# Kernel tuning notes

Measured on AMD Instinct MI355X. Metric: run time of the kernel, lower is better.

## Reference

```python
import jax, jax.numpy as jnp
import numpy as np

B, L, D = 4, 64, 512          # batch, trajectory length, d_model
DI, N, DC, R = 1024, 16, 4, 32  # d_inner, d_state, d_conv, dt_rank
NL = 4                         # n_layers
SD, AD, MEL = 17, 6, 1000      # state_dim, act_dim, max_ep_len
EPS = 1e-5


def setup_inputs() -> dict:
    key = jax.random.key(0)
    ks = iter(jax.random.split(key, 40))
    nrm = lambda shp, s=0.02: jax.random.normal(next(ks), shp, jnp.float32) * s
    inp = {
        "states": jax.random.normal(next(ks), (B, L, SD), jnp.float32),
        "actions": jax.random.normal(next(ks), (B, L, AD), jnp.float32),
        "returns_to_go": jax.random.normal(next(ks), (B, L, 1), jnp.float32),
        "constraints_to_go": jax.random.normal(next(ks), (B, L, 1), jnp.float32),
        "timesteps": jax.random.randint(next(ks), (B, L), 0, MEL, jnp.int32),
        # embedding / projection heads (torch Linear: y = x @ W.T + b)
        "es_w": nrm((D, SD)), "es_b": jnp.zeros((D,), jnp.float32),
        "ea_w": nrm((D, AD)), "ea_b": jnp.zeros((D,), jnp.float32),
        "er_w": nrm((D, 1)), "er_b": jnp.zeros((D,), jnp.float32),
        "ec_w": nrm((D, 1)), "ec_b": jnp.zeros((D,), jnp.float32),
        "et_w": nrm((MEL, D)),
        # per-layer Mamba params, stacked on leading NL axis
        "ln_w": jnp.ones((NL, D), jnp.float32), "ln_b": jnp.zeros((NL, D), jnp.float32),
        "in_w": nrm((NL, 2 * DI, D)),
        "conv_w": nrm((NL, DI, DC), 0.1), "conv_b": jnp.zeros((NL, DI), jnp.float32),
        "xp_w": nrm((NL, R + 2 * N, DI)),
        "dtp_w": nrm((NL, DI, R), 0.1),
        "dtp_b": jnp.full((NL, DI), -4.6, jnp.float32) + nrm((NL, DI), 0.1),
        "A_log": jnp.broadcast_to(jnp.log(jnp.arange(1, N + 1, dtype=jnp.float32)), (NL, DI, N)) * jnp.ones((NL, DI, 1), jnp.float32),
        "Dp": jnp.ones((NL, DI), jnp.float32),
        "out_w": nrm((NL, D, DI)),
        # final norm + heads
        "fn_w": jnp.ones((D,), jnp.float32), "fn_b": jnp.zeros((D,), jnp.float32),
        "ps_w": nrm((SD, D)), "ps_b": jnp.zeros((SD,), jnp.float32),
        "pa_w": nrm((AD, D)), "pa_b": jnp.zeros((AD,), jnp.float32),
    }
    return inp


def layernorm(x, w, b):
    mu = jnp.mean(x, -1, keepdims=True)
    var = jnp.mean(jnp.square(x - mu), -1, keepdims=True)
    return (x - mu) * jax.lax.rsqrt(var + EPS) * w + b


def selective_scan(u, delta, A, Bm, Cm, Dp):
    # u, delta: (B,T,DI); A: (DI,N); Bm, Cm: (B,T,N); Dp: (DI,)
    dA = jnp.exp(delta[..., None] * A)                      # (B,T,DI,N)
    dBu = delta[..., None] * Bm[:, :, None, :] * u[..., None]

    def step(h, xs):
        dA_t, dBu_t, C_t = xs
        h = dA_t * h + dBu_t                                # (B,DI,N)
        y = jnp.einsum('bdn,bn->bd', h, C_t)
        return h, y

    h0 = jnp.zeros((u.shape[0], u.shape[2], A.shape[1]), u.dtype)
    xs = (dA.transpose(1, 0, 2, 3), dBu.transpose(1, 0, 2, 3), Cm.transpose(1, 0, 2))
    _, ys = jax.lax.scan(step, h0, xs)
    return ys.transpose(1, 0, 2) + u * Dp


def mamba_mixer(x, in_w, conv_w, conv_b, xp_w, dtp_w, dtp_b, A_log, Dp, out_w):
    T = x.shape[1]
    xz = x @ in_w.T                                         # (B,T,2*DI)
    xm, z = jnp.split(xz, 2, axis=-1)
    # causal depthwise conv1d, kernel DC
    xpad = jnp.pad(xm, ((0, 0), (DC - 1, 0), (0, 0)))
    xc = sum(xpad[:, k:k + T, :] * conv_w[:, k] for k in range(DC)) + conv_b
    xc = jax.nn.silu(xc)
    dbc = xc @ xp_w.T                                       # (B,T,R+2N)
    dt, Bm, Cm = jnp.split(dbc, [R, R + N], axis=-1)
    delta = jax.nn.softplus(dt @ dtp_w.T + dtp_b)           # (B,T,DI)
    y = selective_scan(xc, delta, -jnp.exp(A_log), Bm, Cm, Dp)
    y = y * jax.nn.silu(z)
    return y @ out_w.T


def reference(states, actions, returns_to_go, constraints_to_go, timesteps,
              es_w, es_b, ea_w, ea_b, er_w, er_b, ec_w, ec_b, et_w,
              ln_w, ln_b, in_w, conv_w, conv_b, xp_w, dtp_w, dtp_b, A_log, Dp, out_w,
              fn_w, fn_b, ps_w, ps_b, pa_w, pa_b):
    te = et_w[timesteps]                                    # (B,L,D)
    se = states @ es_w.T + es_b + te
    ae = actions @ ea_w.T + ea_b + te
    re = returns_to_go @ er_w.T + er_b + te
    ce = constraints_to_go @ ec_w.T + ec_b + te
    # interleave (r, c, s, a) per timestep -> (B, 4L, D)
    x = jnp.stack((re, ce, se, ae), axis=2).reshape(B, 4 * L, D)
    for i in range(NL):
        x = x + mamba_mixer(layernorm(x, ln_w[i], ln_b[i]),
                            in_w[i], conv_w[i], conv_b[i], xp_w[i],
                            dtp_w[i], dtp_b[i], A_log[i], Dp[i], out_w[i])
    x = layernorm(x, fn_w, fn_b)
    outputs = x.reshape(B, L, 4, D).transpose(0, 2, 1, 3)   # (B,4,L,D)
    state_preds = outputs[:, 3] @ ps_w.T + ps_b             # from action tokens
    action_preds = outputs[:, 2] @ pa_w.T + pa_b            # from state tokens
    return state_preds, action_preds
```

## Files before the change

kernel.cpp:

```cpp
#include <hip/hip_runtime.h>
#include <math.h>

#define B_ 4
#define L_ 64
#define D_ 512
#define DI_ 1024
#define N_ 16
#define DC_ 4
#define R_ 32
#define NL_ 4
#define SD_ 17
#define AD_ 6
#define T_ 256
#define CH3_ 32
#define TC3_ 8
#define DL3_ 8

#define NW_IN  (NL_ * 2 * DI_ * D_)
#define NW_OUT (NL_ * D_ * DI_)
#define NW_XP  (NL_ * 64 * DI_)
#define NW_TOT (NW_IN + NW_OUT + NW_XP)
#define WCVT_BLOCKS (NW_TOT / 4 / 256)

typedef short bf16x8 __attribute__((ext_vector_type(8)));
typedef float f32x4 __attribute__((ext_vector_type(4)));

__device__ __forceinline__ float silu_f(float v) { return v / (1.f + __expf(-v)); }
__device__ __forceinline__ float softplus_f(float v) {
    return fmaxf(v, 0.f) + log1pf(__expf(-fabsf(v)));
}
__device__ __forceinline__ unsigned short f2bs(float f) {
    unsigned u = __float_as_uint(f);
    u += 0x7fffu + ((u >> 16) & 1u);
    return (unsigned short)(u >> 16);
}
__device__ __forceinline__ float bs2f(unsigned short s) {
    return __uint_as_float(((unsigned)s) << 16);
}

__global__ __launch_bounds__(256) void init_kernel(
    const float* __restrict__ in_w, const float* __restrict__ out_w,
    const float* __restrict__ xp_w, unsigned short* __restrict__ wb,
    const float* __restrict__ states, const float* __restrict__ actions,
    const float* __restrict__ rtg, const float* __restrict__ ctg,
    const int* __restrict__ ts,
    const float* __restrict__ es_w, const float* __restrict__ es_b,
    const float* __restrict__ ea_w, const float* __restrict__ ea_b,
    const float* __restrict__ er_w, const float* __restrict__ er_b,
    const float* __restrict__ ec_w, const float* __restrict__ ec_b,
    const float* __restrict__ et_w, float* __restrict__ x)
{
    if (blockIdx.x < WCVT_BLOCKS) {
        const int i = blockIdx.x * 256 + threadIdx.x;
        const int e = i * 4;
        const float* src; int off;
        if (e < NW_IN)               { src = in_w;  off = e; }
        else if (e < NW_IN + NW_OUT) { src = out_w; off = e - NW_IN; }
        else                         { src = xp_w;  off = e - NW_IN - NW_OUT; }
        const float4 v = *(const float4*)(src + off);
        ushort4 o;
        o.x = f2bs(v.x); o.y = f2bs(v.y); o.z = f2bs(v.z); o.w = f2bs(v.w);
        *(ushort4*)(wb + e) = o;
    } else {
        const int bl = blockIdx.x - WCVT_BLOCKS;
#pragma unroll
        for (int j = 0; j < 2; ++j) {
            const int d = threadIdx.x + j * 256;
            const float te = et_w[(size_t)ts[bl] * D_ + d];
            const float r = rtg[bl] * er_w[d] + er_b[d] + te;
            const float c = ctg[bl] * ec_w[d] + ec_b[d] + te;
            float s = es_b[d] + te;
#pragma unroll
            for (int k = 0; k < SD_; ++k) s += states[bl * SD_ + k] * es_w[d * SD_ + k];
            float a = ea_b[d] + te;
#pragma unroll
            for (int k = 0; k < AD_; ++k) a += actions[bl * AD_ + k] * ea_w[d * AD_ + k];
            float* xp = x + (size_t)bl * 4 * D_;
            xp[0 * D_ + d] = r;
            xp[1 * D_ + d] = c;
            xp[2 * D_ + d] = s;
            xp[3 * D_ + d] = a;
        }
    }
}

template <int MODE>
__global__ __launch_bounds__(256) void ln2_kernel(
    float* __restrict__ x, const float* __restrict__ p0,
    const float* __restrict__ p1,
    const float* __restrict__ w, const float* __restrict__ b,
    void* __restrict__ o_)
{
    const int tok = blockIdx.x;
    const int tid = threadIdx.x;
    float2 v = reinterpret_cast<float2*>(x + (size_t)tok * D_)[tid];
    if (MODE >= 1) {
        const float2 a0 = reinterpret_cast<const float2*>(p0 + (size_t)tok * D_)[tid];
        const float2 a1 = reinterpret_cast<const float2*>(p1 + (size_t)tok * D_)[tid];
        v.x += a0.x + a1.x;
        v.y += a0.y + a1.y;
        reinterpret_cast<float2*>(x + (size_t)tok * D_)[tid] = v;
    }
    float s = v.x + v.y;
#pragma unroll
    for (int off = 1; off < 64; off <<= 1) s += __shfl_xor(s, off);
    __shared__ float red[8];
    const int wv = tid >> 6;
    if ((tid & 63) == 0) red[wv] = s;
    __syncthreads();
    const float mean = (red[0] + red[1] + red[2] + red[3]) * (1.f / D_);
    const float dx = v.x - mean, dy = v.y - mean;
    float q = dx * dx + dy * dy;
#pragma unroll
    for (int off = 1; off < 64; off <<= 1) q += __shfl_xor(q, off);
    if ((tid & 63) == 0) red[4 + wv] = q;
    __syncthreads();
    const float var = (red[4] + red[5] + red[6] + red[7]) * (1.f / D_);
    const float r = rsqrtf(var + 1e-5f);
    const int d0 = tid * 2;
    const float o0 = dx * r * w[d0] + b[d0];
    const float o1 = dy * r * w[d0 + 1] + b[d0 + 1];
    if (MODE == 2) {
        float* o = (float*)o_;
        o[(size_t)tok * D_ + d0] = o0;
        o[(size_t)tok * D_ + d0 + 1] = o1;
    } else {
        unsigned short* o = (unsigned short*)o_;
        o[(size_t)tok * D_ + d0] = f2bs(o0);
        o[(size_t)tok * D_ + d0 + 1] = f2bs(o1);
    }
}

__global__ __launch_bounds__(256) void inproj_kernel(
    const unsigned short* __restrict__ A, const unsigned short* __restrict__ W,
    const float* __restrict__ cw, const float* __restrict__ cb,
    unsigned short* __restrict__ xcb, unsigned short* __restrict__ zs)
{
    __shared__ unsigned short sxm[80][72];
    const int lane = threadIdx.x & 63, wid = threadIdx.x >> 6;
    const int r = lane & 15, kq = lane >> 4;
    const int m0 = blockIdx.y * 64;
    const int n0 = blockIdx.x * 64;
    const bool is_xm = (n0 < DI_);
    const int wm = m0 + (wid >> 1) * 32;
    const int wn = n0 + (wid & 1) * 32;
    f32x4 acc[2][2] = {};
    f32x4 accx[2] = {};
    int xrow = m0 - 16 + r;
    if (xrow < 0) xrow = 0;
#pragma unroll 4
    for (int k0 = 0; k0 < D_; k0 += 32) {
        bf16x8 a[2], b[2];
#pragma unroll
        for (int i = 0; i < 2; ++i)
            a[i] = *(const bf16x8*)(A + (size_t)(wm + i * 16 + r) * D_ + k0 + kq * 8);
#pragma unroll
        for (int j = 0; j < 2; ++j)
            b[j] = *(const bf16x8*)(W + (size_t)(wn + j * 16 + r) * D_ + k0 + kq * 8);
#pragma unroll
        for (int i = 0; i < 2; ++i)
#pragma unroll
            for (int j = 0; j < 2; ++j)
                acc[i][j] = __builtin_amdgcn_mfma_f32_16x16x32_bf16(a[i], b[j], acc[i][j], 0, 0, 0);
        if (is_xm) {
            const bf16x8 ax = *(const bf16x8*)(A + (size_t)xrow * D_ + k0 + kq * 8);
#pragma unroll
            for (int j = 0; j < 2; ++j)
                accx[j] = __builtin_amdgcn_mfma_f32_16x16x32_bf16(ax, b[j], accx[j], 0, 0, 0);
        }
    }
    if (!is_xm) {
#pragma unroll
        for (int i = 0; i < 2; ++i)
#pragma unroll
            for (int j = 0; j < 2; ++j)
#pragma unroll
                for (int g = 0; g < 4; ++g) {
                    const int row = wm + i * 16 + kq * 4 + g;
                    const int col = wn + j * 16 + r - DI_;
                    zs[(size_t)row * DI_ + col] = f2bs(silu_f(acc[i][j][g]));
                }
        return;
    }
#pragma unroll
    for (int i = 0; i < 2; ++i)
#pragma unroll
        for (int j = 0; j < 2; ++j)
#pragma unroll
            for (int g = 0; g < 4; ++g) {
                const int srow = 16 + (wm - m0) + i * 16 + kq * 4 + g;
                const int scol = (wn - n0) + j * 16 + r;
                sxm[srow][scol] = f2bs(acc[i][j][g]);
            }
#pragma unroll
    for (int j = 0; j < 2; ++j)
#pragma unroll
        for (int g = 0; g < 4; ++g) {
            const int srow = kq * 4 + g;
            const int scol = (wn - n0) + j * 16 + r;
            sxm[srow][scol] = f2bs(accx[j][g]);
        }
    __syncthreads();
    for (int e = threadIdx.x; e < 64 * 64; e += 256) {
        const int col = e & 63, rrel = e >> 6;
        const int grow = m0 + rrel;
        const int t = grow & (T_ - 1);
        const int d = n0 + col;
        const float4 w4 = ((const float4*)cw)[d];
        float a = cb[d];
#pragma unroll
        for (int k = 0; k < DC_; ++k) {
            if (t - 3 + k >= 0) {
                const float wk = (k == 0) ? w4.x : (k == 1) ? w4.y
                               : (k == 2) ? w4.z : w4.w;
                a += wk * bs2f(sxm[16 + rrel - 3 + k][col]);
            }
        }
        xcb[(size_t)grow * DI_ + d] = f2bs(silu_f(a));
    }
}

__global__ __launch_bounds__(256) void xp_kernel(
    const unsigned short* __restrict__ xcb, const unsigned short* __restrict__ Wb,
    float* __restrict__ dbc)
{
    __shared__ float red[4][16][64];
    const int tid = threadIdx.x;
    const int wid = tid >> 6, lane = tid & 63;
    const int r = lane & 15, kq = lane >> 4;
    const int m0 = blockIdx.x * 16;
    f32x4 acc4[4] = {};
    const int k00 = wid * 256;
#pragma unroll
    for (int ks = 0; ks < 8; ++ks) {
        const int k0 = k00 + ks * 32;
        const bf16x8 a = *(const bf16x8*)(xcb + (size_t)(m0 + r) * DI_ + k0 + kq * 8);
#pragma unroll
        for (int j = 0; j < 4; ++j) {
            const bf16x8 bfr = *(const bf16x8*)(Wb + (size_t)(j * 16 + r) * DI_ + k0 + kq * 8);
            acc4[j] = __builtin_amdgcn_mfma_f32_16x16x32_bf16(a, bfr, acc4[j], 0, 0, 0);
        }
    }
#pragma unroll
    for (int j = 0; j < 4; ++j)
#pragma unroll
        for (int g = 0; g < 4; ++g)
            red[wid][kq * 4 + g][j * 16 + r] = acc4[j][g];
    __syncthreads();
    for (int i = tid; i < 1024; i += 256) {
        const int row = i >> 6, col = i & 63;
        const float s = red[0][row][col] + red[1][row][col] +
                        red[2][row][col] + red[3][row][col];
        dbc[(size_t)(m0 + row) * 64 + col] = s;
    }
}

__global__ __launch_bounds__(256, 3) void scan_kernel(
    const unsigned short* __restrict__ xcb, const float* __restrict__ dbc,
    const float* __restrict__ dtw, const float* __restrict__ dtbias,
    const float* __restrict__ A_log, const float* __restrict__ Dp,
    const unsigned short* __restrict__ zs, unsigned short* __restrict__ ygb)
{
    __shared__ float dlt_s[T_][DL3_ + 1];
    __shared__ float Sl[CH3_][DL3_][17];
    __shared__ float Pl[CH3_][DL3_][17];
    const int tid = threadIdx.x;
    const int dl = tid & (DL3_ - 1);
    const int c = tid >> 3;
    const int b = blockIdx.x >> 7;
    const int d = (blockIdx.x & 127) * DL3_ + dl;
    const int row0 = b * T_ + c * TC3_;
    {
        const float4* Wp = (const float4*)(dtw + (size_t)d * R_);
        float4 w4[8];
#pragma unroll
        for (int q = 0; q < 8; ++q) w4[q] = Wp[q];
        const float bias = dtbias[d];
#pragma unroll
        for (int t = 0; t < TC3_; ++t) {
            const float4* Ap = (const float4*)(dbc + (size_t)(row0 + t) * 64);
            float acc = bias;
#pragma unroll
            for (int q = 0; q < 8; ++q) {
                const float4 a4 = Ap[q];
                acc += a4.x * w4[q].x + a4.y * w4[q].y + a4.z * w4[q].z + a4.w * w4[q].w;
            }
            dlt_s[c * TC3_ + t][dl] = softplus_f(acc);
        }
    }
    float Av[N_];
    {
        const float4* Alp = (const float4*)(A_log + (size_t)d * N_);
#pragma unroll
        for (int q = 0; q < 4; ++q) {
            const float4 v = Alp[q];
            Av[q * 4 + 0] = -__expf(v.x);
            Av[q * 4 + 1] = -__expf(v.y);
            Av[q * 4 + 2] = -__expf(v.z);
            Av[q * 4 + 3] = -__expf(v.w);
        }
    }
    __syncthreads();
    const unsigned short* up = xcb + (size_t)row0 * DI_ + d;
    const float* bc = dbc + (size_t)row0 * 64;
    float h[N_];
#pragma unroll
    for (int n = 0; n < N_; ++n) h[n] = 0.f;
    float dsum = 0.f;
#pragma unroll
    for (int t = 0; t < TC3_; ++t) {
        const float dt_t = dlt_s[c * TC3_ + t][dl];
        dsum += dt_t;
        const float dbu = dt_t * bs2f(up[t * DI_]);
#pragma unroll
        for (int q = 0; q < 4; ++q) {
            const float4 b4 = *(const float4*)(bc + t * 64 + R_ + q * 4);
            h[q * 4 + 0] = __expf(dt_t * Av[q * 4 + 0]) * h[q * 4 + 0] + dbu * b4.x;
            h[q * 4 + 1] = __expf(dt_t * Av[q * 4 + 1]) * h[q * 4 + 1] + dbu * b4.y;
            h[q * 4 + 2] = __expf(dt_t * Av[q * 4 + 2]) * h[q * 4 + 2] + dbu * b4.z;
            h[q * 4 + 3] = __expf(dt_t * Av[q * 4 + 3]) * h[q * 4 + 3] + dbu * b4.w;
        }
    }
#pragma unroll
    for (int n = 0; n < N_; ++n) {
        Sl[c][dl][n] = h[n];
        Pl[c][dl][n] = __expf(Av[n] * dsum);
    }
    __syncthreads();
    if (tid < DL3_ * N_) {
        const int dd = tid >> 4, nn = tid & 15;
        float hin = 0.f;
#pragma unroll
        for (int c2 = 0; c2 < CH3_; ++c2) {
            const float t2 = Pl[c2][dd][nn] * hin + Sl[c2][dd][nn];
            Sl[c2][dd][nn] = hin;
            hin = t2;
        }
    }
    __syncthreads();
#pragma unroll
    for (int n = 0; n < N_; ++n) h[n] = Sl[c][dl][n];
    const float Dd = Dp[d];
    const unsigned short* zp = zs + (size_t)row0 * DI_ + d;
    unsigned short* yp = ygb + (size_t)row0 * DI_ + d;
#pragma unroll
    for (int t = 0; t < TC3_; ++t) {
        const float dt_t = dlt_s[c * TC3_ + t][dl];
        const float ut = bs2f(up[t * DI_]);
        const float dbu = dt_t * ut;
        float y = ut * Dd;
#pragma unroll
        for (int q = 0; q < 4; ++q) {
            const float4 b4 = *(const float4*)(bc + t * 64 + R_ + q * 4);
            const float4 c4 = *(const float4*)(bc + t * 64 + R_ + N_ + q * 4);
            h[q * 4 + 0] = __expf(dt_t * Av[q * 4 + 0]) * h[q * 4 + 0] + dbu * b4.x;
            h[q * 4 + 1] = __expf(dt_t * Av[q * 4 + 1]) * h[q * 4 + 1] + dbu * b4.y;
            h[q * 4 + 2] = __expf(dt_t * Av[q * 4 + 2]) * h[q * 4 + 2] + dbu * b4.z;
            h[q * 4 + 3] = __expf(dt_t * Av[q * 4 + 3]) * h[q * 4 + 3] + dbu * b4.w;
            y += h[q * 4 + 0] * c4.x + h[q * 4 + 1] * c4.y
               + h[q * 4 + 2] * c4.z + h[q * 4 + 3] * c4.w;
        }
        yp[t * DI_] = f2bs(y * bs2f(zp[t * DI_]));
    }
}

__global__ __launch_bounds__(256) void outproj_kernel(
    const unsigned short* __restrict__ A, const unsigned short* __restrict__ W,
    float* __restrict__ p)
{
    const int lane = threadIdx.x & 63, wid = threadIdx.x >> 6;
    const int r = lane & 15, kq = lane >> 4;
    const int wm = blockIdx.y * 64 + (wid >> 1) * 32;
    const int wn = blockIdx.x * 64 + (wid & 1) * 32;
    const int kb = blockIdx.z * 512;
    f32x4 acc[2][2] = {};
#pragma unroll 4
    for (int k0 = 0; k0 < 512; k0 += 32) {
        bf16x8 a[2], b[2];
#pragma unroll
        for (int i = 0; i < 2; ++i)
            a[i] = *(const bf16x8*)(A + (size_t)(wm + i * 16 + r) * DI_ + kb + k0 + kq * 8);
#pragma unroll
        for (int j = 0; j < 2; ++j)
            b[j] = *(const bf16x8*)(W + (size_t)(wn + j * 16 + r) * DI_ + kb + k0 + kq * 8);
#pragma unroll
        for (int i = 0; i < 2; ++i)
#pragma unroll
            for (int j = 0; j < 2; ++j)
                acc[i][j] = __builtin_amdgcn_mfma_f32_16x16x32_bf16(a[i], b[j], acc[i][j], 0, 0, 0);
    }
#pragma unroll
    for (int i = 0; i < 2; ++i)
#pragma unroll
        for (int j = 0; j < 2; ++j)
#pragma unroll
            for (int g = 0; g < 4; ++g) {
                const int row = wm + i * 16 + kq * 4 + g;
                const int col = wn + j * 16 + r;
                p[(size_t)blockIdx.z * (1024 * 512) + (size_t)row * 512 + col] = acc[i][j][g];
            }
}

__global__ __launch_bounds__(256) void heads_kernel(
    const float* __restrict__ xn,
    const float* __restrict__ ps_w, const float* __restrict__ ps_b,
    const float* __restrict__ pa_w, const float* __restrict__ pa_b,
    float* __restrict__ out)
{
    const int idx = blockIdx.x * 4 + (threadIdx.x >> 6);
    const int lane = threadIdx.x & 63;
    const int bl = idx / 23, j = idx % 23;
    const float* tok;
    const float* wrow;
    float bias;
    float* dst;
    if (j < SD_) {
        tok = xn + ((size_t)bl * 4 + 3) * D_;
        wrow = ps_w + (size_t)j * D_;
        bias = ps_b[j];
        dst = out + (size_t)bl * SD_ + j;
    } else {
        const int jj = j - SD_;
        tok = xn + ((size_t)bl * 4 + 2) * D_;
        wrow = pa_w + (size_t)jj * D_;
        bias = pa_b[jj];
        dst = out + (size_t)B_ * L_ * SD_ + (size_t)bl * AD_ + jj;
    }
    float s = 0.f;
    for (int dd = lane; dd < D_; dd += 64) s += tok[dd] * wrow[dd];
#pragma unroll
    for (int off = 1; off < 64; off <<= 1) s += __shfl_xor(s, off);
    if (lane == 0) *dst = s + bias;
}

extern "C" void kernel_launch(void* const* d_in, const int* in_sizes, int n_in,
                              void* d_out, int out_size, void* d_ws, size_t ws_size,
                              hipStream_t stream)
{
    const float* states  = (const float*)d_in[0];
    const float* actions = (const float*)d_in[1];
    const float* rtg     = (const float*)d_in[2];
    const float* ctg     = (const float*)d_in[3];
    const int*   ts      = (const int*)d_in[4];
    const float* es_w = (const float*)d_in[5];  const float* es_b = (const float*)d_in[6];
    const float* ea_w = (const float*)d_in[7];  const float* ea_b = (const float*)d_in[8];
    const float* er_w = (const float*)d_in[9];  const float* er_b = (const float*)d_in[10];
    const float* ec_w = (const float*)d_in[11]; const float* ec_b = (const float*)d_in[12];
    const float* et_w = (const float*)d_in[13];
    const float* ln_w = (const float*)d_in[14]; const float* ln_b = (const float*)d_in[15];
    const float* in_w = (const float*)d_in[16];
    const float* conv_w = (const float*)d_in[17]; const float* conv_b = (const float*)d_in[18];
    const float* xp_w = (const float*)d_in[19];
    const float* dtp_w = (const float*)d_in[20]; const float* dtp_b = (const float*)d_in[21];
    const float* A_log = (const float*)d_in[22]; const float* Dp = (const float*)d_in[23];
    const float* out_w = (const float*)d_in[24];
    const float* fn_w = (const float*)d_in[25]; const float* fn_b = (const float*)d_in[26];
    const float* ps_w = (const float*)d_in[27]; const float* ps_b = (const float*)d_in[28];
    const float* pa_w = (const float*)d_in[29]; const float* pa_b = (const float*)d_in[30];
    float* out = (float*)d_out;

    float* ws   = (float*)d_ws;
    float* x    = ws;
    float* xn   = x + 524288;
    float* p    = xn + 524288;
    float* dbc  = p + 1048576;
    unsigned short* xnb = (unsigned short*)(dbc + 65536);
    unsigned short* xcb = xnb + 524288;
    unsigned short* zs  = xcb + 1048576;
    unsigned short* ygb = zs + 1048576;
    unsigned short* wb  = ygb + 1048576;
    unsigned short* wb_in  = wb;
    unsigned short* wb_out = wb + NW_IN;
    unsigned short* wb_xp  = wb + NW_IN + NW_OUT;

    init_kernel<<<WCVT_BLOCKS + B_ * L_, 256, 0, stream>>>(
        in_w, out_w, xp_w, wb,
        states, actions, rtg, ctg, ts,
        es_w, es_b, ea_w, ea_b, er_w, er_b, ec_w, ec_b, et_w, x);

    for (int i = 0; i < NL_; ++i) {
        if (i == 0)
            ln2_kernel<0><<<B_ * T_, 256, 0, stream>>>(
                x, nullptr, nullptr, ln_w, ln_b, xnb);
        else
            ln2_kernel<1><<<B_ * T_, 256, 0, stream>>>(
                x, p, p + 524288, ln_w + i * D_, ln_b + i * D_, xnb);
        inproj_kernel<<<dim3(32, 16), 256, 0, stream>>>(
            xnb, wb_in + (size_t)i * 2 * DI_ * D_,
            conv_w + i * DI_ * DC_, conv_b + i * DI_, xcb, zs);
        xp_kernel<<<64, 256, 0, stream>>>(
            xcb, wb_xp + (size_t)i * 64 * DI_, dbc);
        scan_kernel<<<B_ * (DI_ / DL3_), 256, 0, stream>>>(
            xcb, dbc, dtp_w + (size_t)i * DI_ * R_, dtp_b + i * DI_,
            A_log + (size_t)i * DI_ * N_, Dp + i * DI_, zs, ygb);
        outproj_kernel<<<dim3(8, 16, 2), 256, 0, stream>>>(
            ygb, wb_out + (size_t)i * D_ * DI_, p);
    }

    ln2_kernel<2><<<B_ * T_, 256, 0, stream>>>(x, p, p + 524288, fn_w, fn_b, xn);
    heads_kernel<<<(B_ * L_ * 23) / 4, 256, 0, stream>>>(xn, ps_w, ps_b, pa_w, pa_b, out);
}
```

Measured before the change: 287.3 us.

## Stage scan inputs u, z and B/C in shared memory before chunked scan

The scan kernel now cooperatively loads each block's u and z bf16 columns and the B/C rows of dbc into padded shared-memory tiles. The two sequential passes then read from LDS instead of issuing strided 2-byte global loads and repeated float4 reads. The Sl/Pl carry buffers reuse the bc_s array, so B/C is reloaded from global after the carry propagation. The larger LDS footprint lowers the launch-bounds occupancy hint from 3 to 2 blocks per CU and adds extra barriers.

```diff
diff --git a/kernel.cpp b/kernel.cpp
--- a/kernel.cpp
+++ b/kernel.cpp
@@ -255,21 +255,35 @@
     }
 }
 
-__global__ __launch_bounds__(256, 3) void scan_kernel(
+__global__ __launch_bounds__(256, 2) void scan_kernel(
     const unsigned short* __restrict__ xcb, const float* __restrict__ dbc,
     const float* __restrict__ dtw, const float* __restrict__ dtbias,
     const float* __restrict__ A_log, const float* __restrict__ Dp,
     const unsigned short* __restrict__ zs, unsigned short* __restrict__ ygb)
 {
     __shared__ float dlt_s[T_][DL3_ + 1];
-    __shared__ float Sl[CH3_][DL3_][17];
-    __shared__ float Pl[CH3_][DL3_][17];
+    __shared__ float u_s[T_][DL3_ + 1];
+    __shared__ float z_s[T_][DL3_ + 1];
+    __shared__ float bc_s[T_ * 33];
     const int tid = threadIdx.x;
     const int dl = tid & (DL3_ - 1);
     const int c = tid >> 3;
     const int b = blockIdx.x >> 7;
-    const int d = (blockIdx.x & 127) * DL3_ + dl;
+    const int dband = blockIdx.x & 127;
+    const int d = dband * DL3_ + dl;
+    const int d0 = dband * DL3_;
     const int row0 = b * T_ + c * TC3_;
+
+    for (int i = tid; i < T_ * DL3_; i += 256) {
+        const int t = i >> 3, dd = i & 7;
+        const size_t g = (size_t)(b * T_ + t) * DI_ + d0 + dd;
+        u_s[t][dd] = bs2f(xcb[g]);
+        z_s[t][dd] = bs2f(zs[g]);
+    }
+    for (int i = tid; i < T_ * 32; i += 256) {
+        const int t = i >> 5, j = i & 31;
+        bc_s[t * 33 + j] = dbc[(size_t)(b * T_ + t) * 64 + R_ + j];
+    }
     {
         const float4* Wp = (const float4*)(dtw + (size_t)d * R_);
         float4 w4[8];
@@ -301,66 +315,88 @@
         }
     }
     __syncthreads();
-    const unsigned short* up = xcb + (size_t)row0 * DI_ + d;
-    const float* bc = dbc + (size_t)row0 * 64;
     float h[N_];
 #pragma unroll
     for (int n = 0; n < N_; ++n) h[n] = 0.f;
     float dsum = 0.f;
 #pragma unroll
     for (int t = 0; t < TC3_; ++t) {
-        const float dt_t = dlt_s[c * TC3_ + t][dl];
+        const int tg = c * TC3_ + t;
+        const float dt_t = dlt_s[tg][dl];
         dsum += dt_t;
-        const float dbu = dt_t * bs2f(up[t * DI_]);
+        const float dbu = dt_t * u_s[tg][dl];
 #pragma unroll
         for (int q = 0; q < 4; ++q) {
-            const float4 b4 = *(const float4*)(bc + t * 64 + R_ + q * 4);
-            h[q * 4 + 0] = __expf(dt_t * Av[q * 4 + 0]) * h[q * 4 + 0] + dbu * b4.x;
-            h[q * 4 + 1] = __expf(dt_t * Av[q * 4 + 1]) * h[q * 4 + 1] + dbu * b4.y;
-            h[q * 4 + 2] = __expf(dt_t * Av[q * 4 + 2]) * h[q * 4 + 2] + dbu * b4.z;
-            h[q * 4 + 3] = __expf(dt_t * Av[q * 4 + 3]) * h[q * 4 + 3] + dbu * b4.w;
-        }
-    }
-#pragma unroll
-    for (int n = 0; n < N_; ++n) {
-        Sl[c][dl][n] = h[n];
-        Pl[c][dl][n] = __expf(Av[n] * dsum);
+            const float b0 = bc_s[tg * 33 + q * 4 + 0];
+            const float b1 = bc_s[tg * 33 + q * 4 + 1];
+            const float b2 = bc_s[tg * 33 + q * 4 + 2];
+            const float b3 = bc_s[tg * 33 + q * 4 + 3];
+            h[q * 4 + 0] = __expf(dt_t * Av[q * 4 + 0]) * h[q * 4 + 0] + dbu * b0;
+            h[q * 4 + 1] = __expf(dt_t * Av[q * 4 + 1]) * h[q * 4 + 1] + dbu * b1;
+            h[q * 4 + 2] = __expf(dt_t * Av[q * 4 + 2]) * h[q * 4 + 2] + dbu * b2;
+            h[q * 4 + 3] = __expf(dt_t * Av[q * 4 + 3]) * h[q * 4 + 3] + dbu * b3;
+        }
+    }
+    __syncthreads();
+    {
+        float* Sl = bc_s;
+        float* Pl = bc_s + 4096;
+#pragma unroll
+        for (int n = 0; n < N_; ++n) {
+            Sl[(c * DL3_ + dl) * N_ + n] = h[n];
+            Pl[(c * DL3_ + dl) * N_ + n] = __expf(Av[n] * dsum);
+        }
     }
     __syncthreads();
     if (tid < DL3_ * N_) {
+        float* Sl = bc_s;
+        float* Pl = bc_s + 4096;
         const int dd = tid >> 4, nn = tid & 15;
         float hin = 0.f;
 #pragma unroll
         for (int c2 = 0; c2 < CH3_; ++c2) {
-            const float t2 = Pl[c2][dd][nn] * hin + Sl[c2][dd][nn];
-            Sl[c2][dd][nn] = hin;
+            const int idx = (c2 * DL3_ + dd) * N_ + nn;
+            const float t2 = Pl[idx] * hin + Sl[idx];
+            Sl[idx] = hin;
             hin = t2;
         }
     }
     __syncthreads();
 #pragma unroll
-    for (int n = 0; n < N_; ++n) h[n] = Sl[c][dl][n];
+    for (int n = 0; n < N_; ++n) h[n] = bc_s[(c * DL3_ + dl) * N_ + n];
+    __syncthreads();
+    for (int i = tid; i < T_ * 32; i += 256) {
+        const int t = i >> 5, j = i & 31;
+        bc_s[t * 33 + j] = dbc[(size_t)(b * T_ + t) * 64 + R_ + j];
+    }
+    __syncthreads();
     const float Dd = Dp[d];
-    const unsigned short* zp = zs + (size_t)row0 * DI_ + d;
     unsigned short* yp = ygb + (size_t)row0 * DI_ + d;
 #pragma unroll
     for (int t = 0; t < TC3_; ++t) {
-        const float dt_t = dlt_s[c * TC3_ + t][dl];
-        const float ut = bs2f(up[t * DI_]);
+        const int tg = c * TC3_ + t;
+        const float dt_t = dlt_s[tg][dl];
+        const float ut = u_s[tg][dl];
         const float dbu = dt_t * ut;
         float y = ut * Dd;
 #pragma unroll
         for (int q = 0; q < 4; ++q) {
-            const float4 b4 = *(const float4*)(bc + t * 64 + R_ + q * 4);
-            const float4 c4 = *(const float4*)(bc + t * 64 + R_ + N_ + q * 4);
-            h[q * 4 + 0] = __expf(dt_t * Av[q * 4 + 0]) * h[q * 4 + 0] + dbu * b4.x;
-            h[q * 4 + 1] = __expf(dt_t * Av[q * 4 + 1]) * h[q * 4 + 1] + dbu * b4.y;
-            h[q * 4 + 2] = __expf(dt_t * Av[q * 4 + 2]) * h[q * 4 + 2] + dbu * b4.z;
-            h[q * 4 + 3] = __expf(dt_t * Av[q * 4 + 3]) * h[q * 4 + 3] + dbu * b4.w;
-            y += h[q * 4 + 0] * c4.x + h[q * 4 + 1] * c4.y
-               + h[q * 4 + 2] * c4.z + h[q * 4 + 3] * c4.w;
-        }
-        yp[t * DI_] = f2bs(y * bs2f(zp[t * DI_]));
+            const float b0 = bc_s[tg * 33 + q * 4 + 0];
+            const float b1 = bc_s[tg * 33 + q * 4 + 1];
+            const float b2 = bc_s[tg * 33 + q * 4 + 2];
+            const float b3 = bc_s[tg * 33 + q * 4 + 3];
+            const float c0 = bc_s[tg * 33 + 16 + q * 4 + 0];
+            const float c1 = bc_s[tg * 33 + 16 + q * 4 + 1];
+            const float c2 = bc_s[tg * 33 + 16 + q * 4 + 2];
+            const float c3 = bc_s[tg * 33 + 16 + q * 4 + 3];
+            h[q * 4 + 0] = __expf(dt_t * Av[q * 4 + 0]) * h[q * 4 + 0] + dbu * b0;
+            h[q * 4 + 1] = __expf(dt_t * Av[q * 4 + 1]) * h[q * 4 + 1] + dbu * b1;
+            h[q * 4 + 2] = __expf(dt_t * Av[q * 4 + 2]) * h[q * 4 + 2] + dbu * b2;
+            h[q * 4 + 3] = __expf(dt_t * Av[q * 4 + 3]) * h[q * 4 + 3] + dbu * b3;
+            y += h[q * 4 + 0] * c0 + h[q * 4 + 1] * c1
+               + h[q * 4 + 2] * c2 + h[q * 4 + 3] * c3;
+        }
+        yp[t * DI_] = f2bs(y * z_s[tg][dl]);
     }
 }
 
```

Result: slower. 300.4 us (+4.6%).

## Split selective scan into three kernels with global chunk-state exchange

Applied to the files above, without the earlier changes.

The single block-local scan kernel is replaced by three launches: per-chunk local scans that write chunk states, decay products and deltas to global memory, a cross-chunk prefix kernel, and a final pass that rescans with the carried-in states. Each block now covers 256 channels of one chunk, so the dt projection and the B/C reads are shared across more channels and the serialized in-block cross-chunk step goes away. In exchange it adds two launches per layer and around 20 MB of global traffic per layer for the S/P/delta buffers. The P/S layout in the cross-chunk kernel is strided with a 64 KB step per chunk.

```diff
diff --git a/kernel.cpp b/kernel.cpp
--- a/kernel.cpp
+++ b/kernel.cpp
@@ -14,7 +14,6 @@
 #define T_ 256
 #define CH3_ 32
 #define TC3_ 8
-#define DL3_ 8
 
 #define NW_IN  (NL_ * 2 * DI_ * D_)
 #define NW_OUT (NL_ * D_ * DI_)
@@ -255,39 +254,25 @@
     }
 }
 
-__global__ __launch_bounds__(256, 3) void scan_kernel(
+__global__ __launch_bounds__(256) void scan_p1_kernel(
     const unsigned short* __restrict__ xcb, const float* __restrict__ dbc,
     const float* __restrict__ dtw, const float* __restrict__ dtbias,
-    const float* __restrict__ A_log, const float* __restrict__ Dp,
-    const unsigned short* __restrict__ zs, unsigned short* __restrict__ ygb)
-{
-    __shared__ float dlt_s[T_][DL3_ + 1];
-    __shared__ float Sl[CH3_][DL3_][17];
-    __shared__ float Pl[CH3_][DL3_][17];
+    const float* __restrict__ A_log,
+    float* __restrict__ Sg, float* __restrict__ Pg, float* __restrict__ dltg)
+{
     const int tid = threadIdx.x;
-    const int dl = tid & (DL3_ - 1);
-    const int c = tid >> 3;
     const int b = blockIdx.x >> 7;
-    const int d = (blockIdx.x & 127) * DL3_ + dl;
+    const int c = (blockIdx.x >> 2) & 31;
+    const int dband = blockIdx.x & 3;
+    const int d = dband * 256 + tid;
     const int row0 = b * T_ + c * TC3_;
+    float4 w4[8];
     {
         const float4* Wp = (const float4*)(dtw + (size_t)d * R_);
-        float4 w4[8];
 #pragma unroll
         for (int q = 0; q < 8; ++q) w4[q] = Wp[q];
-        const float bias = dtbias[d];
-#pragma unroll
-        for (int t = 0; t < TC3_; ++t) {
-            const float4* Ap = (const float4*)(dbc + (size_t)(row0 + t) * 64);
-            float acc = bias;
-#pragma unroll
-            for (int q = 0; q < 8; ++q) {
-                const float4 a4 = Ap[q];
-                acc += a4.x * w4[q].x + a4.y * w4[q].y + a4.z * w4[q].z + a4.w * w4[q].w;
-            }
-            dlt_s[c * TC3_ + t][dl] = softplus_f(acc);
-        }
-    }
+    }
+    const float bias = dtbias[d];
     float Av[N_];
     {
         const float4* Alp = (const float4*)(A_log + (size_t)d * N_);
@@ -300,59 +285,104 @@
             Av[q * 4 + 3] = -__expf(v.w);
         }
     }
-    __syncthreads();
-    const unsigned short* up = xcb + (size_t)row0 * DI_ + d;
-    const float* bc = dbc + (size_t)row0 * 64;
     float h[N_];
 #pragma unroll
     for (int n = 0; n < N_; ++n) h[n] = 0.f;
     float dsum = 0.f;
 #pragma unroll
     for (int t = 0; t < TC3_; ++t) {
-        const float dt_t = dlt_s[c * TC3_ + t][dl];
+        const int row = row0 + t;
+        const float4* Ap = (const float4*)(dbc + (size_t)row * 64);
+        float acc = bias;
+#pragma unroll
+        for (int q = 0; q < 8; ++q) {
+            const float4 a4 = Ap[q];
+            acc += a4.x * w4[q].x + a4.y * w4[q].y + a4.z * w4[q].z + a4.w * w4[q].w;
+        }
+        const float dt_t = softplus_f(acc);
+        dltg[(size_t)row * DI_ + d] = dt_t;
         dsum += dt_t;
-        const float dbu = dt_t * bs2f(up[t * DI_]);
+        const float dbu = dt_t * bs2f(xcb[(size_t)row * DI_ + d]);
 #pragma unroll
         for (int q = 0; q < 4; ++q) {
-            const float4 b4 = *(const float4*)(bc + t * 64 + R_ + q * 4);
+            const float4 b4 = Ap[8 + q];
             h[q * 4 + 0] = __expf(dt_t * Av[q * 4 + 0]) * h[q * 4 + 0] + dbu * b4.x;
             h[q * 4 + 1] = __expf(dt_t * Av[q * 4 + 1]) * h[q * 4 + 1] + dbu * b4.y;
             h[q * 4 + 2] = __expf(dt_t * Av[q * 4 + 2]) * h[q * 4 + 2] + dbu * b4.z;
             h[q * 4 + 3] = __expf(dt_t * Av[q * 4 + 3]) * h[q * 4 + 3] + dbu * b4.w;
         }
     }
+    const size_t base = (((size_t)b * CH3_ + c) * DI_ + d) * N_;
 #pragma unroll
     for (int n = 0; n < N_; ++n) {
-        Sl[c][dl][n] = h[n];
-        Pl[c][dl][n] = __expf(Av[n] * dsum);
-    }
-    __syncthreads();
-    if (tid < DL3_ * N_) {
-        const int dd = tid >> 4, nn = tid & 15;
-        float hin = 0.f;
-#pragma unroll
-        for (int c2 = 0; c2 < CH3_; ++c2) {
-            const float t2 = Pl[c2][dd][nn] * hin + Sl[c2][dd][nn];
-            Sl[c2][dd][nn] = hin;
-            hin = t2;
-        }
-    }
-    __syncthreads();
-#pragma unroll
-    for (int n = 0; n < N_; ++n) h[n] = Sl[c][dl][n];
+        Sg[base + n] = h[n];
+        Pg[base + n] = __expf(Av[n] * dsum);
+    }
+}
+
+__global__ __launch_bounds__(256) void scan_p2_kernel(
+    const float* __restrict__ Pg, float* __restrict__ Sg)
+{
+    const int i = blockIdx.x * 256 + threadIdx.x;
+    const int b = i >> 14;
+    const int dn = i & 16383;
+    float hcur = 0.f;
+#pragma unroll
+    for (int c = 0; c < CH3_; ++c) {
+        const size_t idx = ((size_t)b * CH3_ + c) * (DI_ * N_) + dn;
+        const float t2 = Pg[idx] * hcur + Sg[idx];
+        Sg[idx] = hcur;
+        hcur = t2;
+    }
+}
+
+__global__ __launch_bounds__(256) void scan_p3_kernel(
+    const unsigned short* __restrict__ xcb, const float* __restrict__ dbc,
+    const float* __restrict__ dltg, const float* __restrict__ A_log,
+    const float* __restrict__ Dp, const float* __restrict__ Sg,
+    const unsigned short* __restrict__ zs, unsigned short* __restrict__ ygb)
+{
+    const int tid = threadIdx.x;
+    const int b = blockIdx.x >> 7;
+    const int c = (blockIdx.x >> 2) & 31;
+    const int dband = blockIdx.x & 3;
+    const int d = dband * 256 + tid;
+    const int row0 = b * T_ + c * TC3_;
+    float Av[N_];
+    {
+        const float4* Alp = (const float4*)(A_log + (size_t)d * N_);
+#pragma unroll
+        for (int q = 0; q < 4; ++q) {
+            const float4 v = Alp[q];
+            Av[q * 4 + 0] = -__expf(v.x);
+            Av[q * 4 + 1] = -__expf(v.y);
+            Av[q * 4 + 2] = -__expf(v.z);
+            Av[q * 4 + 3] = -__expf(v.w);
+        }
+    }
+    float h[N_];
+    {
+        const size_t base = (((size_t)b * CH3_ + c) * DI_ + d) * N_;
+#pragma unroll
+        for (int q = 0; q < 4; ++q) {
+            const float4 v = *(const float4*)(Sg + base + q * 4);
+            h[q * 4 + 0] = v.x; h[q * 4 + 1] = v.y;
+            h[q * 4 + 2] = v.z; h[q * 4 + 3] = v.w;
+        }
+    }
     const float Dd = Dp[d];
-    const unsigned short* zp = zs + (size_t)row0 * DI_ + d;
-    unsigned short* yp = ygb + (size_t)row0 * DI_ + d;
 #pragma unroll
     for (int t = 0; t < TC3_; ++t) {
-        const float dt_t = dlt_s[c * TC3_ + t][dl];
-        const float ut = bs2f(up[t * DI_]);
+        const int row = row0 + t;
+        const float dt_t = dltg[(size_t)row * DI_ + d];
+        const float ut = bs2f(xcb[(size_t)row * DI_ + d]);
         const float dbu = dt_t * ut;
+        const float4* Ap = (const float4*)(dbc + (size_t)row * 64);
         float y = ut * Dd;
 #pragma unroll
         for (int q = 0; q < 4; ++q) {
-            const float4 b4 = *(const float4*)(bc + t * 64 + R_ + q * 4);
-            const float4 c4 = *(const float4*)(bc + t * 64 + R_ + N_ + q * 4);
+            const float4 b4 = Ap[8 + q];
+            const float4 c4 = Ap[12 + q];
             h[q * 4 + 0] = __expf(dt_t * Av[q * 4 + 0]) * h[q * 4 + 0] + dbu * b4.x;
             h[q * 4 + 1] = __expf(dt_t * Av[q * 4 + 1]) * h[q * 4 + 1] + dbu * b4.y;
             h[q * 4 + 2] = __expf(dt_t * Av[q * 4 + 2]) * h[q * 4 + 2] + dbu * b4.z;
@@ -360,7 +390,7 @@
             y += h[q * 4 + 0] * c4.x + h[q * 4 + 1] * c4.y
                + h[q * 4 + 2] * c4.z + h[q * 4 + 3] * c4.w;
         }
-        yp[t * DI_] = f2bs(y * bs2f(zp[t * DI_]));
+        ygb[(size_t)row * DI_ + d] = f2bs(y * bs2f(zs[(size_t)row * DI_ + d]));
     }
 }
 
@@ -464,7 +494,10 @@
     float* xn   = x + 524288;
     float* p    = xn + 524288;
     float* dbc  = p + 1048576;
-    unsigned short* xnb = (unsigned short*)(dbc + 65536);
+    float* Sg   = dbc + 65536;
+    float* Pg   = Sg + 2097152;
+    float* dltg = Pg + 2097152;
+    unsigned short* xnb = (unsigned short*)(dltg + 1048576);
     unsigned short* xcb = xnb + 524288;
     unsigned short* zs  = xcb + 1048576;
     unsigned short* ygb = zs + 1048576;
@@ -490,9 +523,13 @@
             conv_w + i * DI_ * DC_, conv_b + i * DI_, xcb, zs);
         xp_kernel<<<64, 256, 0, stream>>>(
             xcb, wb_xp + (size_t)i * 64 * DI_, dbc);
-        scan_kernel<<<B_ * (DI_ / DL3_), 256, 0, stream>>>(
+        scan_p1_kernel<<<512, 256, 0, stream>>>(
             xcb, dbc, dtp_w + (size_t)i * DI_ * R_, dtp_b + i * DI_,
-            A_log + (size_t)i * DI_ * N_, Dp + i * DI_, zs, ygb);
+            A_log + (size_t)i * DI_ * N_, Sg, Pg, dltg);
+        scan_p2_kernel<<<256, 256, 0, stream>>>(Pg, Sg);
+        scan_p3_kernel<<<512, 256, 0, stream>>>(
+            xcb, dbc, dltg, A_log + (size_t)i * DI_ * N_,
+            Dp + i * DI_, Sg, zs, ygb);
         outproj_kernel<<<dim3(8, 16, 2), 256, 0, stream>>>(
             ygb, wb_out + (size_t)i * D_ * DI_, p);
     }
```

New measurement: 344.7 us. 20.0% more time.

## Write transposed conv output and gate for scan to read with vector loads

Applied to the files above, without the earlier changes.

The in-projection kernel now also writes the conv output and the SiLU gate in a channel-major (transposed, padded) layout, going through shared memory. The scan kernel then loads its 8 timesteps of u and z per channel with one 16-byte vector load each, instead of strided scalar loads across rows. This trades extra shared-memory staging and an extra global write of xcb for more coalesced scan-side reads. The row-major xcb is kept because xp_kernel still reads it.

```diff
diff --git a/kernel.cpp b/kernel.cpp
--- a/kernel.cpp
+++ b/kernel.cpp
@@ -15,6 +15,7 @@
 #define CH3_ 32
 #define TC3_ 8
 #define DL3_ 8
+#define XTS_ 1032
 
 #define NW_IN  (NL_ * 2 * DI_ * D_)
 #define NW_OUT (NL_ * D_ * DI_)
@@ -134,9 +135,11 @@
 __global__ __launch_bounds__(256) void inproj_kernel(
     const unsigned short* __restrict__ A, const unsigned short* __restrict__ W,
     const float* __restrict__ cw, const float* __restrict__ cb,
-    unsigned short* __restrict__ xcb, unsigned short* __restrict__ zs)
+    unsigned short* __restrict__ xcb, unsigned short* __restrict__ xcbT,
+    unsigned short* __restrict__ zsT)
 {
     __shared__ unsigned short sxm[80][72];
+    __shared__ unsigned short conv_s[64][72];
     const int lane = threadIdx.x & 63, wid = threadIdx.x >> 6;
     const int r = lane & 15, kq = lane >> 4;
     const int m0 = blockIdx.y * 64;
@@ -176,10 +179,23 @@
             for (int j = 0; j < 2; ++j)
 #pragma unroll
                 for (int g = 0; g < 4; ++g) {
-                    const int row = wm + i * 16 + kq * 4 + g;
-                    const int col = wn + j * 16 + r - DI_;
-                    zs[(size_t)row * DI_ + col] = f2bs(silu_f(acc[i][j][g]));
+                    const int lrow = (wm - m0) + i * 16 + kq * 4 + g;
+                    const int lcol = (wn - n0) + j * 16 + r;
+                    sxm[lrow][lcol] = f2bs(silu_f(acc[i][j][g]));
                 }
+        __syncthreads();
+        {
+            const int dcol = threadIdx.x >> 2, tq = threadIdx.x & 3;
+            bf16x8 v0, v1;
+#pragma unroll
+            for (int j = 0; j < 8; ++j) {
+                v0[j] = (short)sxm[tq * 16 + j][dcol];
+                v1[j] = (short)sxm[tq * 16 + 8 + j][dcol];
+            }
+            unsigned short* dst = zsT + (size_t)(n0 - DI_ + dcol) * XTS_ + m0 + tq * 16;
+            *(bf16x8*)dst = v0;
+            *(bf16x8*)(dst + 8) = v1;
+        }
         return;
     }
 #pragma unroll
@@ -216,7 +232,22 @@
                 a += wk * bs2f(sxm[16 + rrel - 3 + k][col]);
             }
         }
-        xcb[(size_t)grow * DI_ + d] = f2bs(silu_f(a));
+        const unsigned short ov = f2bs(silu_f(a));
+        xcb[(size_t)grow * DI_ + d] = ov;
+        conv_s[rrel][col] = ov;
+    }
+    __syncthreads();
+    {
+        const int dcol = threadIdx.x >> 2, tq = threadIdx.x & 3;
+        bf16x8 v0, v1;
+#pragma unroll
+        for (int j = 0; j < 8; ++j) {
+            v0[j] = (short)conv_s[tq * 16 + j][dcol];
+            v1[j] = (short)conv_s[tq * 16 + 8 + j][dcol];
+        }
+        unsigned short* dst = xcbT + (size_t)(n0 + dcol) * XTS_ + m0 + tq * 16;
+        *(bf16x8*)dst = v0;
+        *(bf16x8*)(dst + 8) = v1;
     }
 }
 
@@ -256,10 +287,10 @@
 }
 
 __global__ __launch_bounds__(256, 3) void scan_kernel(
-    const unsigned short* __restrict__ xcb, const float* __restrict__ dbc,
+    const unsigned short* __restrict__ xcbT, const float* __restrict__ dbc,
     const float* __restrict__ dtw, const float* __restrict__ dtbias,
     const float* __restrict__ A_log, const float* __restrict__ Dp,
-    const unsigned short* __restrict__ zs, unsigned short* __restrict__ ygb)
+    const unsigned short* __restrict__ zsT, unsigned short* __restrict__ ygb)
 {
     __shared__ float dlt_s[T_][DL3_ + 1];
     __shared__ float Sl[CH3_][DL3_][17];
@@ -270,6 +301,7 @@
     const int b = blockIdx.x >> 7;
     const int d = (blockIdx.x & 127) * DL3_ + dl;
     const int row0 = b * T_ + c * TC3_;
+    const bf16x8 uv = *(const bf16x8*)(xcbT + (size_t)d * XTS_ + b * T_ + c * TC3_);
     {
         const float4* Wp = (const float4*)(dtw + (size_t)d * R_);
         float4 w4[8];
@@ -301,7 +333,6 @@
         }
     }
     __syncthreads();
-    const unsigned short* up = xcb + (size_t)row0 * DI_ + d;
     const float* bc = dbc + (size_t)row0 * 64;
     float h[N_];
 #pragma unroll
@@ -311,7 +342,7 @@
     for (int t = 0; t < TC3_; ++t) {
         const float dt_t = dlt_s[c * TC3_ + t][dl];
         dsum += dt_t;
-        const float dbu = dt_t * bs2f(up[t * DI_]);
+        const float dbu = dt_t * bs2f((unsigned short)uv[t]);
 #pragma unroll
         for (int q = 0; q < 4; ++q) {
             const float4 b4 = *(const float4*)(bc + t * 64 + R_ + q * 4);
@@ -341,12 +372,12 @@
 #pragma unroll
     for (int n = 0; n < N_; ++n) h[n] = Sl[c][dl][n];
     const float Dd = Dp[d];
-    const unsigned short* zp = zs + (size_t)row0 * DI_ + d;
+    const bf16x8 zv = *(const bf16x8*)(zsT + (size_t)d * XTS_ + b * T_ + c * TC3_);
     unsigned short* yp = ygb + (size_t)row0 * DI_ + d;
 #pragma unroll
     for (int t = 0; t < TC3_; ++t) {
         const float dt_t = dlt_s[c * TC3_ + t][dl];
-        const float ut = bs2f(up[t * DI_]);
+        const float ut = bs2f((unsigned short)uv[t]);
         const float dbu = dt_t * ut;
         float y = ut * Dd;
 #pragma unroll
@@ -360,7 +391,7 @@
             y += h[q * 4 + 0] * c4.x + h[q * 4 + 1] * c4.y
                + h[q * 4 + 2] * c4.z + h[q * 4 + 3] * c4.w;
         }
-        yp[t * DI_] = f2bs(y * bs2f(zp[t * DI_]));
+        yp[t * DI_] = f2bs(y * bs2f((unsigned short)zv[t]));
     }
 }
 
@@ -464,11 +495,12 @@
     float* xn   = x + 524288;
     float* p    = xn + 524288;
     float* dbc  = p + 1048576;
-    unsigned short* xnb = (unsigned short*)(dbc + 65536);
-    unsigned short* xcb = xnb + 524288;
-    unsigned short* zs  = xcb + 1048576;
-    unsigned short* ygb = zs + 1048576;
-    unsigned short* wb  = ygb + 1048576;
+    unsigned short* xnb  = (unsigned short*)(dbc + 65536);
+    unsigned short* xcb  = xnb + 524288;
+    unsigned short* xcbT = xcb + 1048576;
+    unsigned short* zsT  = xcbT + (size_t)DI_ * XTS_;
+    unsigned short* ygb  = zsT + (size_t)DI_ * XTS_;
+    unsigned short* wb   = ygb + 1048576;
     unsigned short* wb_in  = wb;
     unsigned short* wb_out = wb + NW_IN;
     unsigned short* wb_xp  = wb + NW_IN + NW_OUT;
@@ -487,12 +519,12 @@
                 x, p, p + 524288, ln_w + i * D_, ln_b + i * D_, xnb);
         inproj_kernel<<<dim3(32, 16), 256, 0, stream>>>(
             xnb, wb_in + (size_t)i * 2 * DI_ * D_,
-            conv_w + i * DI_ * DC_, conv_b + i * DI_, xcb, zs);
+            conv_w + i * DI_ * DC_, conv_b + i * DI_, xcb, xcbT, zsT);
         xp_kernel<<<64, 256, 0, stream>>>(
             xcb, wb_xp + (size_t)i * 64 * DI_, dbc);
         scan_kernel<<<B_ * (DI_ / DL3_), 256, 0, stream>>>(
-            xcb, dbc, dtp_w + (size_t)i * DI_ * R_, dtp_b + i * DI_,
-            A_log + (size_t)i * DI_ * N_, Dp + i * DI_, zs, ygb);
+            xcbT, dbc, dtp_w + (size_t)i * DI_ * R_, dtp_b + i * DI_,
+            A_log + (size_t)i * DI_ * N_, Dp + i * DI_, zsT, ygb);
         outproj_kernel<<<dim3(8, 16, 2), 256, 0, stream>>>(
             ygb, wb_out + (size_t)i * D_ * DI_, p);
     }
```

Measured after the change: 287.1 us. No clear change (-0.1%).
